# Optimization experiments

Measured on AMD Instinct MI355X. Metric: run time of the kernel, lower is better.

## Reference

```python
import jax, jax.numpy as jnp
import numpy as np
import math

B, Q, K, D = 16, 2048, 2048, 128


def setup_inputs() -> dict:
    key = jax.random.key(0)
    kq, kk, kv, kl = jax.random.split(key, 4)
    queries = jax.random.normal(kq, (B, Q, D), dtype=jnp.float32)
    keys = jax.random.normal(kk, (B, K, D), dtype=jnp.float32)
    values = jax.random.normal(kv, (B, K, D), dtype=jnp.float32)
    valid_lens = jax.random.randint(kl, (B,), 1, K + 1, dtype=jnp.int32)
    return {"queries": queries, "keys": keys, "values": values, "valid_lens": valid_lens}


def reference(queries, keys, values, valid_lens):
    d = queries.shape[-1]
    # scores = bmm(Q, K^T) // sqrt(d)  -- source uses floor-division, kept faithfully
    scores = jnp.floor(jnp.einsum('bqd,bkd->bqk', queries, keys) / math.sqrt(d))
    # masked_softmax: positions >= valid_len[b] get -1e6 before softmax
    mask = jnp.arange(keys.shape[1]) < valid_lens[:, None, None]  # [B,1,K]
    scores = jnp.where(mask, scores, -1e6)
    attn = jax.nn.softmax(scores, axis=-1)
    # dropout in eval mode = identity
    return jnp.einsum('bqk,bkv->bqv', attn, values)
```

## Files before the change

kernel.cpp:

```cpp
#include <hip/hip_runtime.h>
#include <cmath>

typedef __attribute__((ext_vector_type(4))) float f32x4;
typedef __attribute__((ext_vector_type(8))) _Float16 f16x8;
typedef __attribute__((ext_vector_type(4))) _Float16 f16x4;
typedef __attribute__((ext_vector_type(4))) unsigned int u32x4;

#define B_SZ 16
#define Q_SZ 2048
#define K_SZ 2048
#define D_SZ 128
#define BQ   128
#define BKT  64
#define SCL  0.08838834764831845f

#define GLDS16(g, s) __builtin_amdgcn_global_load_lds(                      \
    (const __attribute__((address_space(1))) unsigned int*)(g),             \
    (__attribute__((address_space(3))) unsigned int*)(s), 16, 0, 0)

static __device__ inline unsigned pk16(float a, float b) {
  unsigned short ha = __builtin_bit_cast(unsigned short, (_Float16)a);
  unsigned short hb = __builtin_bit_cast(unsigned short, (_Float16)b);
  return (unsigned)ha | ((unsigned)hb << 16);
}

__global__ __launch_bounds__(256) void prep_all(
    const float* __restrict__ K, const float* __restrict__ V,
    _Float16* __restrict__ Khi, _Float16* __restrict__ Klo,
    _Float16* __restrict__ Vt)
{
  __shared__ _Float16 tmp[64][136];
  const int tid = threadIdx.x;
  if (blockIdx.x < 2048) {
    const int gid = blockIdx.x * 256 + tid;
    const int r = gid >> 4;
    const int g = gid & 15;
    const float* src = K + (size_t)r * D_SZ + g * 8;
    f16x8 hi, lo;
#pragma unroll
    for (int i = 0; i < 8; ++i) {
      float x = src[i];
      _Float16 h = (_Float16)x;
      hi[i] = h;
      lo[i] = (_Float16)((x - (float)h) * 2048.0f);
    }
    const size_t o = (size_t)r * D_SZ + ((g ^ (r & 7)) * 8);
    *(f16x8*)(Khi + o) = hi;
    *(f16x8*)(Klo + o) = lo;
  } else {
    const int vb = blockIdx.x - 2048;
    const int b = vb >> 5;
    const int k0 = (vb & 31) * 64;
    const float* Vb = V + ((size_t)b * K_SZ + k0) * D_SZ;
#pragma unroll
    for (int j = 0; j < 8; ++j) {
      const int e = j * 1024 + tid * 4;
      const int k = e >> 7, d = e & 127;
      const f32x4 v = *(const f32x4*)(Vb + (size_t)k * D_SZ + d);
      f16x4 h;
#pragma unroll
      for (int i = 0; i < 4; ++i) h[i] = (_Float16)v[i];
      *(f16x4*)&tmp[k][d] = h;
    }
    __syncthreads();
#pragma unroll
    for (int i = 0; i < 4; ++i) {
      const int id = i * 256 + tid;
      const int gk = id >> 7, d = id & 127;
      f16x8 o;
#pragma unroll
      for (int jj = 0; jj < 8; ++jj) {
        const int kap = ((gk >> 2) << 5) | ((jj >> 2) << 4) | ((gk & 3) << 2) | (jj & 3);
        o[jj] = tmp[kap][d];
      }
      _Float16* dst = Vt + ((size_t)b * D_SZ + d) * K_SZ + k0 + ((gk ^ (d & 7)) * 8);
      *(f16x8*)dst = o;
    }
  }
}

__global__ __launch_bounds__(256, 2) void attn(
    const float* __restrict__ Qm, const _Float16* __restrict__ KhiG,
    const _Float16* __restrict__ KloG, const _Float16* __restrict__ VtG,
    const int* __restrict__ vlp, float* __restrict__ Om,
    float* __restrict__ P1, float* __restrict__ L0, float* __restrict__ L1,
    unsigned* __restrict__ cnt, const int split)
{
  __shared__ __align__(16) char sm[65536];
  __shared__ float Ls[128];
  __shared__ int s_task;

  const int tid  = threadIdx.x;
  const int wave = tid >> 6;
  const int lane = tid & 63;
  const int ln   = lane & 15;
  const int quad = lane >> 4;

  for (;;) {
    int t;
    if (split) {
      if (tid == 0) s_task = (int)atomicAdd(cnt, 1u);
      __syncthreads();
      t = s_task;
      __syncthreads();
      if (t >= 512) return;
    } else {
      t = blockIdx.x;
    }

    int half = 0, b, qt;
    if (split) { half = (t >= 256); const int u = t & 255; b = u >> 4; qt = u & 15; }
    else       { b = t >> 4; qt = t & 15; }
    const int q0     = qt * BQ;
    const int valid  = vlp[b];
    const int kstart = half * 1024;
    const int kend   = split ? min(valid, kstart + 1024) : valid;
    if (kend <= kstart) { if (!split) return; continue; }
    const int ntiles = (kend - kstart + BKT - 1) / BKT;

    const float* Qb    = Qm + (size_t)b * Q_SZ * D_SZ;
    const char*  gKhiB = (const char*)KhiG + (size_t)b * K_SZ * 256;
    const char*  gKloB = (const char*)KloG + (size_t)b * K_SZ * 256;
    const char*  gVtB  = (const char*)VtG  + (size_t)b * D_SZ * (K_SZ * 2);

    auto SThi = [&](int k0g, int sel) {
      const char* g = gKhiB + (size_t)k0g * 256;
      char* d = sm + sel * 16384;
#pragma unroll
      for (int i = 0; i < 4; ++i) {
        const int off = wave * 1024 + i * 4096;
        GLDS16(g + off + lane * 16, d + off);
      }
    };
    auto STlo = [&](int k0g) {
      const char* g = gKloB + (size_t)k0g * 256;
      char* d = sm + 32768;
#pragma unroll
      for (int i = 0; i < 4; ++i) {
        const int off = wave * 1024 + i * 4096;
        GLDS16(g + off + lane * 16, d + off);
      }
    };
    auto STv = [&](int k0g) {
      char* dst = sm + 49152;
#pragma unroll
      for (int i = 0; i < 4; ++i) {
        const int off = wave * 1024 + i * 4096;
        const int a = off + lane * 16;
        const int d = a >> 7, win = a & 127;
        GLDS16(gVtB + (size_t)d * (K_SZ * 2) + (size_t)k0g * 2 + win, dst + off);
      }
    };

    f16x8 qhi[2][4], qlo[2][4];
#pragma unroll
    for (int mt = 0; mt < 2; ++mt) {
      const int qrow = q0 + wave * 32 + mt * 16 + ln;
      const float* srcb = Qb + (size_t)qrow * D_SZ + quad * 8;
#pragma unroll
      for (int c = 0; c < 4; ++c) {
#pragma unroll
        for (int j = 0; j < 8; ++j) {
          float x = srcb[c * 32 + j];
          _Float16 h = (_Float16)x;
          qhi[mt][c][j] = h;
          qlo[mt][c][j] = (_Float16)((x - (float)h) * 2048.0f);
        }
      }
    }

    const f32x4 vzero = {0.f, 0.f, 0.f, 0.f};
    f32x4 accO[2][8];
    float lsum[2] = {0.f, 0.f};
#pragma unroll
    for (int mt = 0; mt < 2; ++mt)
#pragma unroll
      for (int dt = 0; dt < 8; ++dt) accO[mt][dt] = vzero;

    SThi(kstart, 0);
    STlo(kstart);

    for (int kt = 0; kt < ntiles; ++kt) {
      const int k0g = kstart + kt * BKT;
      _Float16* smKhi = (_Float16*)(sm + (kt & 1) * 16384);
      _Float16* smKlo = (_Float16*)(sm + 32768);
      _Float16* smVt  = (_Float16*)(sm + 49152);
      const bool more = (kt + 1 < ntiles);

      STv(k0g);
      if (more) {
        SThi(k0g + BKT, (kt + 1) & 1);
        asm volatile("s_waitcnt vmcnt(8)" ::: "memory");
      } else {
        asm volatile("s_waitcnt vmcnt(4)" ::: "memory");
      }
      __builtin_amdgcn_sched_barrier(0);
      __builtin_amdgcn_s_barrier();
      __builtin_amdgcn_sched_barrier(0);

      f16x8 pa[2][2];
#pragma unroll
      for (int hk = 0; hk < 2; ++hk) {
        f32x4 accM[2][2], accC[2][2];
#pragma unroll
        for (int mt = 0; mt < 2; ++mt)
#pragma unroll
          for (int nb2 = 0; nb2 < 2; ++nb2) { accM[mt][nb2] = vzero; accC[mt][nb2] = vzero; }
        __builtin_amdgcn_s_setprio(1);
#pragma unroll
        for (int nb2 = 0; nb2 < 2; ++nb2) {
          const int row = (hk * 2 + nb2) * 16 + ln;
          const _Float16* bh_base = smKhi + row * 128;
          const _Float16* bl_base = smKlo + row * 128;
#pragma unroll
          for (int c = 0; c < 4; ++c) {
            const int pg = (((c * 4 + quad) ^ (ln & 7)) * 8);
            const f16x8 bh = *(const f16x8*)(bh_base + pg);
            const f16x8 bl = *(const f16x8*)(bl_base + pg);
#pragma unroll
            for (int mt = 0; mt < 2; ++mt) {
              accM[mt][nb2] = __builtin_amdgcn_mfma_f32_16x16x32_f16(bh, qhi[mt][c], accM[mt][nb2], 0, 0, 0);
              accC[mt][nb2] = __builtin_amdgcn_mfma_f32_16x16x32_f16(bl, qhi[mt][c], accC[mt][nb2], 0, 0, 0);
              accC[mt][nb2] = __builtin_amdgcn_mfma_f32_16x16x32_f16(bh, qlo[mt][c], accC[mt][nb2], 0, 0, 0);
            }
          }
        }
        __builtin_amdgcn_s_setprio(0);

#pragma unroll
        for (int mt = 0; mt < 2; ++mt) {
          u32x4 w;
#pragma unroll
          for (int nb2 = 0; nb2 < 2; ++nb2) {
            float e[4];
#pragma unroll
            for (int r = 0; r < 4; ++r) {
              const int key = k0g + (hk * 2 + nb2) * 16 + quad * 4 + r;
              const float s = accM[mt][nb2][r] + accC[mt][nb2][r] * (1.0f / 2048.0f);
              e[r] = (key < valid) ? __expf(floorf(s * SCL)) : 0.0f;
              lsum[mt] += e[r];
            }
            w[nb2 * 2 + 0] = pk16(e[0], e[1]);
            w[nb2 * 2 + 1] = pk16(e[2], e[3]);
          }
          pa[mt][hk] = __builtin_bit_cast(f16x8, w);
        }
      }

      if (more) {
        asm volatile("s_waitcnt vmcnt(4)" ::: "memory");
      } else {
        asm volatile("s_waitcnt vmcnt(0)" ::: "memory");
      }
      __builtin_amdgcn_sched_barrier(0);
      __builtin_amdgcn_s_barrier();
      __builtin_amdgcn_sched_barrier(0);
      if (more) STlo(k0g + BKT);

      __builtin_amdgcn_s_setprio(1);
#pragma unroll
      for (int c = 0; c < 2; ++c) {
#pragma unroll
        for (int dt = 0; dt < 8; ++dt) {
          const int drow = dt * 16 + ln;
          const int pg = (((c * 4 + quad) ^ (ln & 7)) * 8);
          const f16x8 bf = *(const f16x8*)(smVt + drow * 64 + pg);
#pragma unroll
          for (int mt = 0; mt < 2; ++mt)
            accO[mt][dt] = __builtin_amdgcn_mfma_f32_16x16x32_f16(pa[mt][c], bf, accO[mt][dt], 0, 0, 0);
        }
      }
      __builtin_amdgcn_s_setprio(0);
      __builtin_amdgcn_sched_barrier(0);
      __builtin_amdgcn_s_barrier();
      __builtin_amdgcn_sched_barrier(0);
    }

#pragma unroll
    for (int mt = 0; mt < 2; ++mt) {
      float v = lsum[mt];
      v += __shfl_xor(v, 16, 64);
      v += __shfl_xor(v, 32, 64);
      lsum[mt] = v;
    }

    if (split) {
      float* Lh = half ? L1 : L0;
      if (lane < 16) {
#pragma unroll
        for (int mt = 0; mt < 2; ++mt)
          atomicAdd(Lh + b * Q_SZ + q0 + wave * 32 + mt * 16 + lane, lsum[mt]);
      }
      float* dst = (half ? P1 : Om) + ((size_t)(b * Q_SZ + q0)) * D_SZ;
#pragma unroll
      for (int mt = 0; mt < 2; ++mt)
#pragma unroll
        for (int dt = 0; dt < 8; ++dt)
#pragma unroll
          for (int r = 0; r < 4; ++r)
            dst[(size_t)(wave * 32 + mt * 16 + quad * 4 + r) * D_SZ + dt * 16 + ln] =
                accO[mt][dt][r];
    } else {
      if (lane < 16) {
#pragma unroll
        for (int mt = 0; mt < 2; ++mt)
          Ls[wave * 32 + mt * 16 + lane] = lsum[mt];
      }
      __syncthreads();
      float* Ob = Om + (size_t)b * Q_SZ * D_SZ;
#pragma unroll
      for (int mt = 0; mt < 2; ++mt) {
#pragma unroll
        for (int r = 0; r < 4; ++r) {
          const float inv = 1.0f / Ls[wave * 32 + mt * 16 + quad * 4 + r];
#pragma unroll
          for (int dt = 0; dt < 8; ++dt)
            Ob[(size_t)(q0 + wave * 32 + mt * 16 + quad * 4 + r) * D_SZ + dt * 16 + ln] =
                accO[mt][dt][r] * inv;
        }
      }
      __syncthreads();
    }
    if (!split) return;
  }
}

__global__ __launch_bounds__(256) void finalize(
    float* __restrict__ Om, const float* __restrict__ P1,
    const float* __restrict__ L0, const float* __restrict__ L1,
    const int* __restrict__ vlp)
{
  const int idx = blockIdx.x * 256 + threadIdx.x;
  const size_t e = (size_t)idx * 4;
  const int row = (int)(e >> 7);
  const int b = row >> 11;
  const int valid = vlp[b];
  f32x4 o = *(const f32x4*)(Om + e);
  float l = L0[row];
  if (valid > 1024) {
    const f32x4 p = *(const f32x4*)(P1 + e);
    o += p;
    l += L1[row];
  }
  const float inv = 1.0f / l;
  o *= inv;
  *(f32x4*)(Om + e) = o;
}

extern "C" void kernel_launch(void* const* d_in, const int* in_sizes, int n_in,
                              void* d_out, int out_size, void* d_ws, size_t ws_size,
                              hipStream_t stream) {
  const float* Qm = (const float*)d_in[0];
  const float* Km = (const float*)d_in[1];
  const float* Vm = (const float*)d_in[2];
  const int*   vl = (const int*)d_in[3];
  float*       Om = (float*)d_out;

  const size_t elems = (size_t)B_SZ * K_SZ * D_SZ;
  const size_t PREP  = 3 * elems * sizeof(_Float16);
  const size_t HDR   = 262400;
  const size_t P1SZ  = elems * sizeof(float);
  char* W = (char*)d_ws;

  if (ws_size >= HDR + PREP + P1SZ) {
    unsigned* cnt = (unsigned*)W;
    float*    L0  = (float*)(W + 256);
    float*    L1  = (float*)(W + 256 + 131072);
    _Float16* Khi = (_Float16*)(W + HDR);
    _Float16* Klo = Khi + elems;
    _Float16* Vt  = Klo + elems;
    float*    P1  = (float*)(W + HDR + PREP);
    hipMemsetAsync(d_ws, 0, HDR, stream);
    prep_all<<<2560, 256, 0, stream>>>(Km, Vm, Khi, Klo, Vt);
    attn<<<512, 256, 0, stream>>>(Qm, Khi, Klo, Vt, vl, Om, P1, L0, L1, cnt, 1);
    finalize<<<4096, 256, 0, stream>>>(Om, P1, L0, L1, vl);
  } else {
    _Float16* Khi = (_Float16*)W;
    _Float16* Klo = Khi + elems;
    _Float16* Vt  = Klo + elems;
    prep_all<<<2560, 256, 0, stream>>>(Km, Vm, Khi, Klo, Vt);
    attn<<<256, 256, 0, stream>>>(Qm, Khi, Klo, Vt, vl, Om,
                                  nullptr, nullptr, nullptr, nullptr, 0);
  }
}
```

Measured before the change: 175.0 us.

## Halve query tile to 64 rows, drop software pipelining, raise occupancy to 3 blocks

Shrinks the query tile from 128 to 64 rows, so each wave handles one 16-row M tile. This halves the accumulator registers and cuts LDS from 64KB to 48KB, which allows 3 blocks per CU. The double-buffered prefetch of K-hi, K-lo and V is replaced with a simple load-all, wait-all, compute loop per key tile, relying on extra occupancy to hide latency. The task count and grid size double or increase accordingly. In exchange, each K/V tile is reloaded twice as often per query, and the explicit load/compute overlap inside a block is lost.

```diff
diff --git a/kernel.cpp b/kernel.cpp
--- a/kernel.cpp
+++ b/kernel.cpp
@@ -10,7 +10,7 @@
 #define Q_SZ 2048
 #define K_SZ 2048
 #define D_SZ 128
-#define BQ   128
+#define BQ   64
 #define BKT  64
 #define SCL  0.08838834764831845f
 
@@ -79,15 +79,15 @@
   }
 }
 
-__global__ __launch_bounds__(256, 2) void attn(
+__global__ __launch_bounds__(256, 3) void attn(
     const float* __restrict__ Qm, const _Float16* __restrict__ KhiG,
     const _Float16* __restrict__ KloG, const _Float16* __restrict__ VtG,
     const int* __restrict__ vlp, float* __restrict__ Om,
     float* __restrict__ P1, float* __restrict__ L0, float* __restrict__ L1,
     unsigned* __restrict__ cnt, const int split)
 {
-  __shared__ __align__(16) char sm[65536];
-  __shared__ float Ls[128];
+  __shared__ __align__(16) char sm[49152];
+  __shared__ float Ls[64];
   __shared__ int s_task;
 
   const int tid  = threadIdx.x;
@@ -95,6 +95,10 @@
   const int lane = tid & 63;
   const int ln   = lane & 15;
   const int quad = lane >> 4;
+
+  _Float16* smKhi = (_Float16*)sm;
+  _Float16* smKlo = (_Float16*)(sm + 16384);
+  _Float16* smVt  = (_Float16*)(sm + 32768);
 
   for (;;) {
     int t;
@@ -103,14 +107,14 @@
       __syncthreads();
       t = s_task;
       __syncthreads();
-      if (t >= 512) return;
+      if (t >= 1024) return;
     } else {
       t = blockIdx.x;
     }
 
     int half = 0, b, qt;
-    if (split) { half = (t >= 256); const int u = t & 255; b = u >> 4; qt = u & 15; }
-    else       { b = t >> 4; qt = t & 15; }
+    if (split) { half = (t >= 512); const int u = t & 511; b = u >> 5; qt = u & 31; }
+    else       { b = t >> 5; qt = t & 31; }
     const int q0     = qt * BQ;
     const int valid  = vlp[b];
     const int kstart = half * 1024;
@@ -123,39 +127,9 @@
     const char*  gKloB = (const char*)KloG + (size_t)b * K_SZ * 256;
     const char*  gVtB  = (const char*)VtG  + (size_t)b * D_SZ * (K_SZ * 2);
 
-    auto SThi = [&](int k0g, int sel) {
-      const char* g = gKhiB + (size_t)k0g * 256;
-      char* d = sm + sel * 16384;
-#pragma unroll
-      for (int i = 0; i < 4; ++i) {
-        const int off = wave * 1024 + i * 4096;
-        GLDS16(g + off + lane * 16, d + off);
-      }
-    };
-    auto STlo = [&](int k0g) {
-      const char* g = gKloB + (size_t)k0g * 256;
-      char* d = sm + 32768;
-#pragma unroll
-      for (int i = 0; i < 4; ++i) {
-        const int off = wave * 1024 + i * 4096;
-        GLDS16(g + off + lane * 16, d + off);
-      }
-    };
-    auto STv = [&](int k0g) {
-      char* dst = sm + 49152;
-#pragma unroll
-      for (int i = 0; i < 4; ++i) {
-        const int off = wave * 1024 + i * 4096;
-        const int a = off + lane * 16;
-        const int d = a >> 7, win = a & 127;
-        GLDS16(gVtB + (size_t)d * (K_SZ * 2) + (size_t)k0g * 2 + win, dst + off);
-      }
-    };
-
-    f16x8 qhi[2][4], qlo[2][4];
-#pragma unroll
-    for (int mt = 0; mt < 2; ++mt) {
-      const int qrow = q0 + wave * 32 + mt * 16 + ln;
+    f16x8 qhi[4], qlo[4];
+    {
+      const int qrow = q0 + wave * 16 + ln;
       const float* srcb = Qb + (size_t)qrow * D_SZ + quad * 8;
 #pragma unroll
       for (int c = 0; c < 4; ++c) {
@@ -163,49 +137,61 @@
         for (int j = 0; j < 8; ++j) {
           float x = srcb[c * 32 + j];
           _Float16 h = (_Float16)x;
-          qhi[mt][c][j] = h;
-          qlo[mt][c][j] = (_Float16)((x - (float)h) * 2048.0f);
+          qhi[c][j] = h;
+          qlo[c][j] = (_Float16)((x - (float)h) * 2048.0f);
         }
       }
     }
 
     const f32x4 vzero = {0.f, 0.f, 0.f, 0.f};
-    f32x4 accO[2][8];
-    float lsum[2] = {0.f, 0.f};
-#pragma unroll
-    for (int mt = 0; mt < 2; ++mt)
-#pragma unroll
-      for (int dt = 0; dt < 8; ++dt) accO[mt][dt] = vzero;
-
-    SThi(kstart, 0);
-    STlo(kstart);
+    f32x4 accO[8];
+    float lsum = 0.0f;
+#pragma unroll
+    for (int dt = 0; dt < 8; ++dt) accO[dt] = vzero;
 
     for (int kt = 0; kt < ntiles; ++kt) {
       const int k0g = kstart + kt * BKT;
-      _Float16* smKhi = (_Float16*)(sm + (kt & 1) * 16384);
-      _Float16* smKlo = (_Float16*)(sm + 32768);
-      _Float16* smVt  = (_Float16*)(sm + 49152);
-      const bool more = (kt + 1 < ntiles);
-
-      STv(k0g);
-      if (more) {
-        SThi(k0g + BKT, (kt + 1) & 1);
-        asm volatile("s_waitcnt vmcnt(8)" ::: "memory");
-      } else {
-        asm volatile("s_waitcnt vmcnt(4)" ::: "memory");
-      }
+
+      if (kt) {
+        asm volatile("s_waitcnt lgkmcnt(0)" ::: "memory");
+        __builtin_amdgcn_sched_barrier(0);
+        __builtin_amdgcn_s_barrier();
+        __builtin_amdgcn_sched_barrier(0);
+      }
+
+      {
+        const char* gh = gKhiB + (size_t)k0g * 256;
+        const char* gl = gKloB + (size_t)k0g * 256;
+#pragma unroll
+        for (int i = 0; i < 4; ++i) {
+          const int off = wave * 1024 + i * 4096;
+          GLDS16(gh + off + lane * 16, sm + off);
+        }
+#pragma unroll
+        for (int i = 0; i < 4; ++i) {
+          const int off = wave * 1024 + i * 4096;
+          GLDS16(gl + off + lane * 16, sm + 16384 + off);
+        }
+#pragma unroll
+        for (int i = 0; i < 4; ++i) {
+          const int off = wave * 1024 + i * 4096;
+          const int a = off + lane * 16;
+          const int d = a >> 7, win = a & 127;
+          GLDS16(gVtB + (size_t)d * (K_SZ * 2) + (size_t)k0g * 2 + win,
+                 sm + 32768 + off);
+        }
+      }
+      asm volatile("s_waitcnt vmcnt(0)" ::: "memory");
       __builtin_amdgcn_sched_barrier(0);
       __builtin_amdgcn_s_barrier();
       __builtin_amdgcn_sched_barrier(0);
 
-      f16x8 pa[2][2];
+      f16x8 pa[2];
 #pragma unroll
       for (int hk = 0; hk < 2; ++hk) {
-        f32x4 accM[2][2], accC[2][2];
-#pragma unroll
-        for (int mt = 0; mt < 2; ++mt)
-#pragma unroll
-          for (int nb2 = 0; nb2 < 2; ++nb2) { accM[mt][nb2] = vzero; accC[mt][nb2] = vzero; }
+        f32x4 accM[2], accC[2];
+#pragma unroll
+        for (int nb2 = 0; nb2 < 2; ++nb2) { accM[nb2] = vzero; accC[nb2] = vzero; }
         __builtin_amdgcn_s_setprio(1);
 #pragma unroll
         for (int nb2 = 0; nb2 < 2; ++nb2) {
@@ -217,45 +203,29 @@
             const int pg = (((c * 4 + quad) ^ (ln & 7)) * 8);
             const f16x8 bh = *(const f16x8*)(bh_base + pg);
             const f16x8 bl = *(const f16x8*)(bl_base + pg);
-#pragma unroll
-            for (int mt = 0; mt < 2; ++mt) {
-              accM[mt][nb2] = __builtin_amdgcn_mfma_f32_16x16x32_f16(bh, qhi[mt][c], accM[mt][nb2], 0, 0, 0);
-              accC[mt][nb2] = __builtin_amdgcn_mfma_f32_16x16x32_f16(bl, qhi[mt][c], accC[mt][nb2], 0, 0, 0);
-              accC[mt][nb2] = __builtin_amdgcn_mfma_f32_16x16x32_f16(bh, qlo[mt][c], accC[mt][nb2], 0, 0, 0);
-            }
+            accM[nb2] = __builtin_amdgcn_mfma_f32_16x16x32_f16(bh, qhi[c], accM[nb2], 0, 0, 0);
+            accC[nb2] = __builtin_amdgcn_mfma_f32_16x16x32_f16(bl, qhi[c], accC[nb2], 0, 0, 0);
+            accC[nb2] = __builtin_amdgcn_mfma_f32_16x16x32_f16(bh, qlo[c], accC[nb2], 0, 0, 0);
           }
         }
         __builtin_amdgcn_s_setprio(0);
 
-#pragma unroll
-        for (int mt = 0; mt < 2; ++mt) {
-          u32x4 w;
-#pragma unroll
-          for (int nb2 = 0; nb2 < 2; ++nb2) {
-            float e[4];
-#pragma unroll
-            for (int r = 0; r < 4; ++r) {
-              const int key = k0g + (hk * 2 + nb2) * 16 + quad * 4 + r;
-              const float s = accM[mt][nb2][r] + accC[mt][nb2][r] * (1.0f / 2048.0f);
-              e[r] = (key < valid) ? __expf(floorf(s * SCL)) : 0.0f;
-              lsum[mt] += e[r];
-            }
-            w[nb2 * 2 + 0] = pk16(e[0], e[1]);
-            w[nb2 * 2 + 1] = pk16(e[2], e[3]);
+        u32x4 w;
+#pragma unroll
+        for (int nb2 = 0; nb2 < 2; ++nb2) {
+          float e[4];
+#pragma unroll
+          for (int r = 0; r < 4; ++r) {
+            const int key = k0g + (hk * 2 + nb2) * 16 + quad * 4 + r;
+            const float s = accM[nb2][r] + accC[nb2][r] * (1.0f / 2048.0f);
+            e[r] = (key < valid) ? __expf(floorf(s * SCL)) : 0.0f;
+            lsum += e[r];
           }
-          pa[mt][hk] = __builtin_bit_cast(f16x8, w);
-        }
-      }
-
-      if (more) {
-        asm volatile("s_waitcnt vmcnt(4)" ::: "memory");
-      } else {
-        asm volatile("s_waitcnt vmcnt(0)" ::: "memory");
-      }
-      __builtin_amdgcn_sched_barrier(0);
-      __builtin_amdgcn_s_barrier();
-      __builtin_amdgcn_sched_barrier(0);
-      if (more) STlo(k0g + BKT);
+          w[nb2 * 2 + 0] = pk16(e[0], e[1]);
+          w[nb2 * 2 + 1] = pk16(e[2], e[3]);
+        }
+        pa[hk] = __builtin_bit_cast(f16x8, w);
+      }
 
       __builtin_amdgcn_s_setprio(1);
 #pragma unroll
@@ -265,61 +235,42 @@
           const int drow = dt * 16 + ln;
           const int pg = (((c * 4 + quad) ^ (ln & 7)) * 8);
           const f16x8 bf = *(const f16x8*)(smVt + drow * 64 + pg);
-#pragma unroll
-          for (int mt = 0; mt < 2; ++mt)
-            accO[mt][dt] = __builtin_amdgcn_mfma_f32_16x16x32_f16(pa[mt][c], bf, accO[mt][dt], 0, 0, 0);
+          accO[dt] = __builtin_amdgcn_mfma_f32_16x16x32_f16(pa[c], bf, accO[dt], 0, 0, 0);
         }
       }
       __builtin_amdgcn_s_setprio(0);
-      __builtin_amdgcn_sched_barrier(0);
-      __builtin_amdgcn_s_barrier();
-      __builtin_amdgcn_sched_barrier(0);
-    }
-
-#pragma unroll
-    for (int mt = 0; mt < 2; ++mt) {
-      float v = lsum[mt];
+    }
+
+    {
+      float v = lsum;
       v += __shfl_xor(v, 16, 64);
       v += __shfl_xor(v, 32, 64);
-      lsum[mt] = v;
+      lsum = v;
     }
 
     if (split) {
       float* Lh = half ? L1 : L0;
-      if (lane < 16) {
-#pragma unroll
-        for (int mt = 0; mt < 2; ++mt)
-          atomicAdd(Lh + b * Q_SZ + q0 + wave * 32 + mt * 16 + lane, lsum[mt]);
-      }
+      if (lane < 16)
+        atomicAdd(Lh + b * Q_SZ + q0 + wave * 16 + lane, lsum);
       float* dst = (half ? P1 : Om) + ((size_t)(b * Q_SZ + q0)) * D_SZ;
 #pragma unroll
-      for (int mt = 0; mt < 2; ++mt)
-#pragma unroll
-        for (int dt = 0; dt < 8; ++dt)
-#pragma unroll
-          for (int r = 0; r < 4; ++r)
-            dst[(size_t)(wave * 32 + mt * 16 + quad * 4 + r) * D_SZ + dt * 16 + ln] =
-                accO[mt][dt][r];
+      for (int dt = 0; dt < 8; ++dt)
+#pragma unroll
+        for (int r = 0; r < 4; ++r)
+          dst[(size_t)(wave * 16 + quad * 4 + r) * D_SZ + dt * 16 + ln] =
+              accO[dt][r];
     } else {
-      if (lane < 16) {
-#pragma unroll
-        for (int mt = 0; mt < 2; ++mt)
-          Ls[wave * 32 + mt * 16 + lane] = lsum[mt];
-      }
+      if (lane < 16) Ls[wave * 16 + lane] = lsum;
       __syncthreads();
       float* Ob = Om + (size_t)b * Q_SZ * D_SZ;
 #pragma unroll
-      for (int mt = 0; mt < 2; ++mt) {
-#pragma unroll
-        for (int r = 0; r < 4; ++r) {
-          const float inv = 1.0f / Ls[wave * 32 + mt * 16 + quad * 4 + r];
-#pragma unroll
-          for (int dt = 0; dt < 8; ++dt)
-            Ob[(size_t)(q0 + wave * 32 + mt * 16 + quad * 4 + r) * D_SZ + dt * 16 + ln] =
-                accO[mt][dt][r] * inv;
-        }
-      }
-      __syncthreads();
+      for (int r = 0; r < 4; ++r) {
+        const float inv = 1.0f / Ls[wave * 16 + quad * 4 + r];
+#pragma unroll
+        for (int dt = 0; dt < 8; ++dt)
+          Ob[(size_t)(q0 + wave * 16 + quad * 4 + r) * D_SZ + dt * 16 + ln] =
+              accO[dt][r] * inv;
+      }
     }
     if (!split) return;
   }
@@ -372,14 +323,14 @@
     float*    P1  = (float*)(W + HDR + PREP);
     hipMemsetAsync(d_ws, 0, HDR, stream);
     prep_all<<<2560, 256, 0, stream>>>(Km, Vm, Khi, Klo, Vt);
-    attn<<<512, 256, 0, stream>>>(Qm, Khi, Klo, Vt, vl, Om, P1, L0, L1, cnt, 1);
+    attn<<<768, 256, 0, stream>>>(Qm, Khi, Klo, Vt, vl, Om, P1, L0, L1, cnt, 1);
     finalize<<<4096, 256, 0, stream>>>(Om, P1, L0, L1, vl);
   } else {
     _Float16* Khi = (_Float16*)W;
     _Float16* Klo = Khi + elems;
     _Float16* Vt  = Klo + elems;
     prep_all<<<2560, 256, 0, stream>>>(Km, Vm, Khi, Klo, Vt);
-    attn<<<256, 256, 0, stream>>>(Qm, Khi, Klo, Vt, vl, Om,
+    attn<<<512, 256, 0, stream>>>(Qm, Khi, Klo, Vt, vl, Om,
                                   nullptr, nullptr, nullptr, nullptr, 0);
   }
 }
```

Result: faster. 164.7 us (-5.8%).

## Split keys into four chunks with atomic accumulation and single-buffered LDS

Applied to the files above, without the earlier changes.

Work items now split the key range into four 512-key chunks instead of two halves, giving 1024 tasks picked up by a 768-block persistent grid. Partial outputs and row sums are combined with float atomics into a pre-zeroed output, which removes the separate P1/L1 buffers and simplifies finalize. LDS shrinks to 48KB with no double buffering so three blocks fit per CU, but each tile now waits for all its loads before computing, so load/compute overlap is lost. The many output atomics add memory traffic and make the summation order nondeterministic.

```diff
diff --git a/kernel.cpp b/kernel.cpp
--- a/kernel.cpp
+++ b/kernel.cpp
@@ -79,14 +79,13 @@
   }
 }
 
-__global__ __launch_bounds__(256, 2) void attn(
+__global__ __launch_bounds__(256, 3) void attn(
     const float* __restrict__ Qm, const _Float16* __restrict__ KhiG,
     const _Float16* __restrict__ KloG, const _Float16* __restrict__ VtG,
     const int* __restrict__ vlp, float* __restrict__ Om,
-    float* __restrict__ P1, float* __restrict__ L0, float* __restrict__ L1,
-    unsigned* __restrict__ cnt, const int split)
+    float* __restrict__ L0, unsigned* __restrict__ cnt, const int split)
 {
-  __shared__ __align__(16) char sm[65536];
+  __shared__ __align__(16) char sm[49152];
   __shared__ float Ls[128];
   __shared__ int s_task;
 
@@ -95,6 +94,10 @@
   const int lane = tid & 63;
   const int ln   = lane & 15;
   const int quad = lane >> 4;
+
+  _Float16* smKhi = (_Float16*)sm;
+  _Float16* smKlo = (_Float16*)(sm + 16384);
+  _Float16* smVt  = (_Float16*)(sm + 32768);
 
   for (;;) {
     int t;
@@ -103,18 +106,18 @@
       __syncthreads();
       t = s_task;
       __syncthreads();
-      if (t >= 512) return;
+      if (t >= 1024) return;
     } else {
       t = blockIdx.x;
     }
 
-    int half = 0, b, qt;
-    if (split) { half = (t >= 256); const int u = t & 255; b = u >> 4; qt = u & 15; }
+    int kq = 0, b, qt;
+    if (split) { kq = t >> 8; const int u = t & 255; b = u >> 4; qt = u & 15; }
     else       { b = t >> 4; qt = t & 15; }
     const int q0     = qt * BQ;
     const int valid  = vlp[b];
-    const int kstart = half * 1024;
-    const int kend   = split ? min(valid, kstart + 1024) : valid;
+    const int kstart = kq * 512;
+    const int kend   = split ? min(valid, kstart + 512) : valid;
     if (kend <= kstart) { if (!split) return; continue; }
     const int ntiles = (kend - kstart + BKT - 1) / BKT;
 
@@ -122,35 +125,6 @@
     const char*  gKhiB = (const char*)KhiG + (size_t)b * K_SZ * 256;
     const char*  gKloB = (const char*)KloG + (size_t)b * K_SZ * 256;
     const char*  gVtB  = (const char*)VtG  + (size_t)b * D_SZ * (K_SZ * 2);
-
-    auto SThi = [&](int k0g, int sel) {
-      const char* g = gKhiB + (size_t)k0g * 256;
-      char* d = sm + sel * 16384;
-#pragma unroll
-      for (int i = 0; i < 4; ++i) {
-        const int off = wave * 1024 + i * 4096;
-        GLDS16(g + off + lane * 16, d + off);
-      }
-    };
-    auto STlo = [&](int k0g) {
-      const char* g = gKloB + (size_t)k0g * 256;
-      char* d = sm + 32768;
-#pragma unroll
-      for (int i = 0; i < 4; ++i) {
-        const int off = wave * 1024 + i * 4096;
-        GLDS16(g + off + lane * 16, d + off);
-      }
-    };
-    auto STv = [&](int k0g) {
-      char* dst = sm + 49152;
-#pragma unroll
-      for (int i = 0; i < 4; ++i) {
-        const int off = wave * 1024 + i * 4096;
-        const int a = off + lane * 16;
-        const int d = a >> 7, win = a & 127;
-        GLDS16(gVtB + (size_t)d * (K_SZ * 2) + (size_t)k0g * 2 + win, dst + off);
-      }
-    };
 
     f16x8 qhi[2][4], qlo[2][4];
 #pragma unroll
@@ -177,23 +151,39 @@
 #pragma unroll
       for (int dt = 0; dt < 8; ++dt) accO[mt][dt] = vzero;
 
-    SThi(kstart, 0);
-    STlo(kstart);
-
     for (int kt = 0; kt < ntiles; ++kt) {
       const int k0g = kstart + kt * BKT;
-      _Float16* smKhi = (_Float16*)(sm + (kt & 1) * 16384);
-      _Float16* smKlo = (_Float16*)(sm + 32768);
-      _Float16* smVt  = (_Float16*)(sm + 49152);
-      const bool more = (kt + 1 < ntiles);
-
-      STv(k0g);
-      if (more) {
-        SThi(k0g + BKT, (kt + 1) & 1);
-        asm volatile("s_waitcnt vmcnt(8)" ::: "memory");
-      } else {
-        asm volatile("s_waitcnt vmcnt(4)" ::: "memory");
-      }
+
+      if (kt) {
+        asm volatile("s_waitcnt lgkmcnt(0)" ::: "memory");
+        __builtin_amdgcn_sched_barrier(0);
+        __builtin_amdgcn_s_barrier();
+        __builtin_amdgcn_sched_barrier(0);
+      }
+
+      {
+        const char* gh = gKhiB + (size_t)k0g * 256;
+        const char* gl = gKloB + (size_t)k0g * 256;
+#pragma unroll
+        for (int i = 0; i < 4; ++i) {
+          const int off = wave * 1024 + i * 4096;
+          GLDS16(gh + off + lane * 16, sm + off);
+        }
+#pragma unroll
+        for (int i = 0; i < 4; ++i) {
+          const int off = wave * 1024 + i * 4096;
+          GLDS16(gl + off + lane * 16, sm + 16384 + off);
+        }
+#pragma unroll
+        for (int i = 0; i < 4; ++i) {
+          const int off = wave * 1024 + i * 4096;
+          const int a = off + lane * 16;
+          const int d = a >> 7, win = a & 127;
+          GLDS16(gVtB + (size_t)d * (K_SZ * 2) + (size_t)k0g * 2 + win,
+                 sm + 32768 + off);
+        }
+      }
+      asm volatile("s_waitcnt vmcnt(0)" ::: "memory");
       __builtin_amdgcn_sched_barrier(0);
       __builtin_amdgcn_s_barrier();
       __builtin_amdgcn_sched_barrier(0);
@@ -247,16 +237,6 @@
         }
       }
 
-      if (more) {
-        asm volatile("s_waitcnt vmcnt(4)" ::: "memory");
-      } else {
-        asm volatile("s_waitcnt vmcnt(0)" ::: "memory");
-      }
-      __builtin_amdgcn_sched_barrier(0);
-      __builtin_amdgcn_s_barrier();
-      __builtin_amdgcn_sched_barrier(0);
-      if (more) STlo(k0g + BKT);
-
       __builtin_amdgcn_s_setprio(1);
 #pragma unroll
       for (int c = 0; c < 2; ++c) {
@@ -271,9 +251,6 @@
         }
       }
       __builtin_amdgcn_s_setprio(0);
-      __builtin_amdgcn_sched_barrier(0);
-      __builtin_amdgcn_s_barrier();
-      __builtin_amdgcn_sched_barrier(0);
     }
 
 #pragma unroll
@@ -285,21 +262,20 @@
     }
 
     if (split) {
-      float* Lh = half ? L1 : L0;
       if (lane < 16) {
 #pragma unroll
         for (int mt = 0; mt < 2; ++mt)
-          atomicAdd(Lh + b * Q_SZ + q0 + wave * 32 + mt * 16 + lane, lsum[mt]);
-      }
-      float* dst = (half ? P1 : Om) + ((size_t)(b * Q_SZ + q0)) * D_SZ;
+          atomicAdd(L0 + b * Q_SZ + q0 + wave * 32 + mt * 16 + lane, lsum[mt]);
+      }
+      float* dst = Om + ((size_t)(b * Q_SZ + q0)) * D_SZ;
 #pragma unroll
       for (int mt = 0; mt < 2; ++mt)
 #pragma unroll
         for (int dt = 0; dt < 8; ++dt)
 #pragma unroll
           for (int r = 0; r < 4; ++r)
-            dst[(size_t)(wave * 32 + mt * 16 + quad * 4 + r) * D_SZ + dt * 16 + ln] =
-                accO[mt][dt][r];
+            atomicAdd(dst + (size_t)(wave * 32 + mt * 16 + quad * 4 + r) * D_SZ + dt * 16 + ln,
+                      accO[mt][dt][r]);
     } else {
       if (lane < 16) {
 #pragma unroll
@@ -319,30 +295,19 @@
                 accO[mt][dt][r] * inv;
         }
       }
-      __syncthreads();
     }
     if (!split) return;
   }
 }
 
 __global__ __launch_bounds__(256) void finalize(
-    float* __restrict__ Om, const float* __restrict__ P1,
-    const float* __restrict__ L0, const float* __restrict__ L1,
-    const int* __restrict__ vlp)
+    float* __restrict__ Om, const float* __restrict__ L0)
 {
   const int idx = blockIdx.x * 256 + threadIdx.x;
   const size_t e = (size_t)idx * 4;
   const int row = (int)(e >> 7);
-  const int b = row >> 11;
-  const int valid = vlp[b];
   f32x4 o = *(const f32x4*)(Om + e);
-  float l = L0[row];
-  if (valid > 1024) {
-    const f32x4 p = *(const f32x4*)(P1 + e);
-    o += p;
-    l += L1[row];
-  }
-  const float inv = 1.0f / l;
+  const float inv = 1.0f / L0[row];
   o *= inv;
   *(f32x4*)(Om + e) = o;
 }
@@ -359,27 +324,25 @@
   const size_t elems = (size_t)B_SZ * K_SZ * D_SZ;
   const size_t PREP  = 3 * elems * sizeof(_Float16);
   const size_t HDR   = 262400;
-  const size_t P1SZ  = elems * sizeof(float);
   char* W = (char*)d_ws;
 
-  if (ws_size >= HDR + PREP + P1SZ) {
+  if (ws_size >= HDR + PREP) {
     unsigned* cnt = (unsigned*)W;
     float*    L0  = (float*)(W + 256);
-    float*    L1  = (float*)(W + 256 + 131072);
     _Float16* Khi = (_Float16*)(W + HDR);
     _Float16* Klo = Khi + elems;
     _Float16* Vt  = Klo + elems;
-    float*    P1  = (float*)(W + HDR + PREP);
     hipMemsetAsync(d_ws, 0, HDR, stream);
+    hipMemsetAsync(d_out, 0, (size_t)out_size, stream);
     prep_all<<<2560, 256, 0, stream>>>(Km, Vm, Khi, Klo, Vt);
-    attn<<<512, 256, 0, stream>>>(Qm, Khi, Klo, Vt, vl, Om, P1, L0, L1, cnt, 1);
-    finalize<<<4096, 256, 0, stream>>>(Om, P1, L0, L1, vl);
+    attn<<<768, 256, 0, stream>>>(Qm, Khi, Klo, Vt, vl, Om, L0, cnt, 1);
+    finalize<<<4096, 256, 0, stream>>>(Om, L0);
   } else {
     _Float16* Khi = (_Float16*)W;
     _Float16* Klo = Khi + elems;
     _Float16* Vt  = Klo + elems;
     prep_all<<<2560, 256, 0, stream>>>(Km, Vm, Khi, Klo, Vt);
     attn<<<256, 256, 0, stream>>>(Qm, Khi, Klo, Vt, vl, Om,
-                                  nullptr, nullptr, nullptr, nullptr, 0);
+                                  nullptr, nullptr, 0);
   }
 }
```

Result: slower. 268.5 us (+53.5%).
